# Optimization experiments

Measured on AMD Instinct MI355X. Metric: run time of the kernel, lower is better.

Reference implementation:

```python
import jax, jax.numpy as jnp
import numpy as np


def conv1x1(x, w, b):
    # x: (B,C,H,W), w: (O,C), b: (O,)
    return jnp.einsum('bchw,oc->bohw', x, w) + b[None, :, None, None]


def maxpool2x2(x):
    B, C, H, W = x.shape
    return x.reshape(B, C, H // 2, 2, W // 2, 2).max(axis=(3, 5))


def setup_inputs() -> dict:
    key = jax.random.key(0)
    ks = jax.random.split(key, 10)
    B, C, H, W = 16, 256, 64, 64
    K = 8
    ck, ch = C // K, C // 2  # 32, 128
    sc = lambda fan_in: 1.0 / np.sqrt(fan_in)
    return {
        'x': jax.random.normal(ks[0], (B, C, H, W), jnp.float32),
        'wf': jax.random.normal(ks[1], (ck, C), jnp.float32) * sc(C),
        'bf': jnp.zeros((ck,), jnp.float32),
        'wg': jax.random.normal(ks[2], (ck, C), jnp.float32) * sc(C),
        'bg': jnp.zeros((ck,), jnp.float32),
        'wh': jax.random.normal(ks[3], (ch, C), jnp.float32) * sc(C),
        'bh': jnp.zeros((ch,), jnp.float32),
        'wv': jax.random.normal(ks[4], (C, ch), jnp.float32) * sc(ch),
        'bv': jnp.zeros((C,), jnp.float32),
        'gamma': jnp.float32(0.5),  # nonzero so the attention branch matters
    }


def reference(x, wf, bf, wg, bg, wh, bh, wv, bv, gamma):
    B, C, H, W = x.shape
    HW = H * W
    f = conv1x1(x, wf, bf).reshape(B, -1, HW)            # (B, C/K, HW)
    g = maxpool2x2(conv1x1(x, wg, bg))                    # (B, C/K, H/2, W/2)
    h = maxpool2x2(conv1x1(x, wh, bh))                    # (B, C/2, H/2, W/2)
    HWp = HW // 4
    g = g.reshape(B, -1, HWp)
    h = h.reshape(B, -1, HWp)
    s = jnp.einsum('bck,bcl->bkl', f, g)                  # (B, HW, HW')
    beta = jax.nn.softmax(s, axis=-1)
    o = jnp.einsum('bjk,blk->bjl', h, beta)               # (B, C/2, HW)
    o = o.reshape(B, -1, H, W)
    return gamma * conv1x1(o, wv, bv) + x
```

## Files before the change

kernel.cpp:

```cpp
#include <hip/hip_runtime.h>
#include <hip/hip_bf16.h>
#include <stdint.h>

#define B_N   16
#define C_N   256
#define W_N   64
#define HW_N  4096
#define CK_N  32
#define CH_N  128
#define HWP_N 1024
#define MR_N  192

typedef __attribute__((ext_vector_type(8))) short short8;
typedef __attribute__((ext_vector_type(4))) float f32x4;
typedef __attribute__((ext_vector_type(4))) unsigned uint4v;

#define MFMA(a, b, c) __builtin_amdgcn_mfma_f32_16x16x32_bf16((a), (b), (c), 0, 0, 0)

__device__ __forceinline__ unsigned short f2bf(float f) {
    union { float f; unsigned u; } v; v.f = f;
    unsigned r = v.u + 0x7FFFu + ((v.u >> 16) & 1u);
    return (unsigned short)(r >> 16);
}
__device__ __forceinline__ unsigned packrn(float lo, float hi) {
    unsigned a = __float_as_uint(lo) + 0x8000u;
    unsigned b = __float_as_uint(hi) + 0x8000u;
    return __builtin_amdgcn_perm(b, a, 0x07060302);
}
__device__ __forceinline__ short8 ld8(const void* p) {
    return *reinterpret_cast<const short8*>(p);
}

__global__ __launch_bounds__(256) void k_prep(
    const float* __restrict__ wf, const float* __restrict__ wg,
    const float* __restrict__ wh, const float* __restrict__ wv,
    unsigned short* __restrict__ Wc, unsigned short* __restrict__ Wv)
{
    int i = blockIdx.x * 256 + threadIdx.x;
    if (i < MR_N * C_N) {
        int r = i / C_N, c = i % C_N;
        float v = (r < 32) ? wf[r * C_N + c]
                : (r < 64) ? wg[(r - 32) * C_N + c]
                           : wh[(r - 64) * C_N + c];
        Wc[i] = f2bf(v);
    }
    if (i < C_N * CH_N) Wv[i] = f2bf(wv[i]);
}

__global__ __launch_bounds__(256) void k_conv_fgh(
    const float* __restrict__ x, const unsigned short* __restrict__ Wc,
    const float* __restrict__ bfp, const float* __restrict__ bgp, const float* __restrict__ bhp,
    unsigned short* __restrict__ f_, unsigned short* __restrict__ g_, unsigned short* __restrict__ h_)
{
    __shared__ __align__(16) unsigned char lds[64 * 512];
    const int T = threadIdx.x;
    const int lane = T & 63, wid = T >> 6;
    const int blk = blockIdx.x;
    const int b = blk >> 6;
    const int seg = blk & 63;
    const int rp = seg >> 1;
    const int half = seg & 1;
    const float* xb = x + (size_t)b * C_N * HW_N;

    #pragma unroll
    for (int i = 0; i < 8; ++i) {
        int task = i * 256 + T;
        int pq = task & 15;
        int cp = task >> 4;
        int px0 = pq * 4;
        int row = 2 * rp + (px0 >> 5);
        int wcol = half * 32 + (px0 & 31);
        const float4 v0 = *reinterpret_cast<const float4*>(xb + (size_t)(2 * cp) * HW_N + row * W_N + wcol);
        const float4 v1 = *reinterpret_cast<const float4*>(xb + (size_t)(2 * cp + 1) * HW_N + row * W_N + wcol);
        float vlo[4] = {v0.x, v0.y, v0.z, v0.w};
        float vhi[4] = {v1.x, v1.y, v1.z, v1.w};
        int kc = cp >> 2, co = cp & 3;
        #pragma unroll
        for (int j = 0; j < 4; ++j) {
            int px = px0 + j;
            *reinterpret_cast<unsigned*>(lds + px * 512 + ((kc ^ (px & 31)) << 4) + co * 4)
                = packrn(vlo[j], vhi[j]);
        }
    }
    __syncthreads();

    const int l15 = lane & 15, quad = lane >> 4;
    f32x4 acc[3][4];
    #pragma unroll
    for (int mt = 0; mt < 3; ++mt)
        #pragma unroll
        for (int nt = 0; nt < 4; ++nt)
            acc[mt][nt] = f32x4{0.f, 0.f, 0.f, 0.f};

    const int m0base = wid * 48;
    for (int k0 = 0; k0 < 256; k0 += 32) {
        short8 afr[3];
        #pragma unroll
        for (int mt = 0; mt < 3; ++mt)
            afr[mt] = ld8(Wc + (size_t)(m0base + mt * 16 + l15) * C_N + k0 + quad * 8);
        #pragma unroll
        for (int nt = 0; nt < 4; ++nt) {
            int px = nt * 16 + l15;
            int kc = (k0 >> 3) + quad;
            short8 bfr = ld8(lds + px * 512 + ((kc ^ (px & 31)) << 4));
            #pragma unroll
            for (int mt = 0; mt < 3; ++mt)
                acc[mt][nt] = MFMA(afr[mt], bfr, acc[mt][nt]);
        }
    }

    #pragma unroll
    for (int mt = 0; mt < 3; ++mt) {
        int mbase = m0base + mt * 16;
        int mrow0 = mbase + quad * 4;
        float bias[4];
        #pragma unroll
        for (int r = 0; r < 4; ++r) {
            int m = mrow0 + r;
            bias[r] = (m < 32) ? bfp[m] : (m < 64) ? bgp[m - 32] : bhp[m - 64];
        }
        if (mbase < 32) {
            #pragma unroll
            for (int nt = 0; nt < 4; ++nt) {
                int px = nt * 16 + l15;
                int p = (2 * rp + (px >> 5)) * W_N + half * 32 + (px & 31);
                uint2 u;
                u.x = packrn(acc[mt][nt][0] + bias[0], acc[mt][nt][1] + bias[1]);
                u.y = packrn(acc[mt][nt][2] + bias[2], acc[mt][nt][3] + bias[3]);
                *reinterpret_cast<uint2*>(f_ + ((size_t)b * HW_N + p) * CK_N + mrow0) = u;
            }
        } else if (mbase < 64) {
            int gc0 = mrow0 - 32;
            #pragma unroll
            for (int nt = 0; nt < 2; ++nt) {
                float pv[4];
                #pragma unroll
                for (int r = 0; r < 4; ++r) {
                    float m1 = fmaxf(acc[mt][nt][r], acc[mt][nt + 2][r]);
                    pv[r] = fmaxf(m1, __shfl_xor(m1, 1)) + bias[r];
                }
                if ((lane & 1) == 0) {
                    int kp = rp * 32 + half * 16 + ((nt * 16 + l15) >> 1);
                    uint2 u;
                    u.x = packrn(pv[0], pv[1]);
                    u.y = packrn(pv[2], pv[3]);
                    *reinterpret_cast<uint2*>(g_ + ((size_t)b * HWP_N + kp) * CK_N + gc0) = u;
                }
            }
        } else {
            int hc0 = mrow0 - 64;
            #pragma unroll
            for (int nt = 0; nt < 2; ++nt) {
                float pv[4];
                #pragma unroll
                for (int r = 0; r < 4; ++r) {
                    float m1 = fmaxf(acc[mt][nt][r], acc[mt][nt + 2][r]);
                    pv[r] = fmaxf(m1, __shfl_xor(m1, 1)) + bias[r];
                }
                #pragma unroll
                for (int r = 0; r < 4; ++r) {
                    int lo = (int)(packrn(pv[r], pv[r]) & 0xFFFFu);
                    int hi = __shfl_down(lo, 2);
                    if ((lane & 3) == 0) {
                        int kp2 = rp * 32 + half * 16 + nt * 8 + (l15 >> 1);
                        *reinterpret_cast<unsigned*>(
                            h_ + ((size_t)b * CH_N + hc0 + r) * HWP_N + kp2)
                            = (unsigned)lo | ((unsigned)hi << 16);
                    }
                }
            }
        }
    }
}

__global__ __launch_bounds__(256, 4) void k_attn(
    const unsigned short* __restrict__ f_, const unsigned short* __restrict__ g_,
    const unsigned short* __restrict__ h_, const unsigned short* __restrict__ Wv,
    const float* __restrict__ bv, const float* __restrict__ x,
    const float* __restrict__ gamma_p, float* __restrict__ out)
{
    __shared__ __align__(16) unsigned char Vl[2 * 17408];
    const int T = threadIdx.x;
    const int lane = T & 63, wid = T >> 6;
    const int l15 = lane & 15, quad = lane >> 4;

    const int blk = blockIdx.x;
    const int b = blk >> 6;
    const int q0w = (blk & 63) * 64 + wid * 16;
    const unsigned short* fb = f_ + (size_t)b * HW_N * CK_N;
    const unsigned short* gb = g_ + (size_t)b * HWP_N * CK_N;
    const unsigned short* hb = h_ + (size_t)b * CH_N * HWP_N;

    short8 ffr = ld8(fb + (size_t)(q0w + l15) * CK_N + quad * 8);

    const f32x4 zf = {0.f, 0.f, 0.f, 0.f};
    f32x4 oacc[8];
    #pragma unroll
    for (int ct = 0; ct < 8; ++ct)
        oacc[ct] = f32x4{0.f, 0.f, 0.f, 0.f};
    float lsum = 0.f;

    const int sch = T >> 3, skq = T & 7;
    const int kq = ((l15 >> 2) << 3) | (l15 & 3);

    uint4 vpre[4];
    #pragma unroll
    for (int i = 0; i < 4; ++i)
        vpre[i] = *reinterpret_cast<const uint4*>(hb + (size_t)(sch + i * 32) * HWP_N + skq * 8);
    short8 gcur[4];
    #pragma unroll
    for (int kt = 0; kt < 4; ++kt)
        gcur[kt] = ld8(gb + (size_t)(((kt >> 1) << 5) + ((kt & 1) << 2) + kq) * CK_N + quad * 8);

    for (int c = 0; c < 16; ++c) {
        unsigned char* buf = Vl + (c & 1) * 17408;
        #pragma unroll
        for (int i = 0; i < 4; ++i) {
            unsigned char* dst = buf + (sch + i * 32) * 136 + skq * 16;
            *reinterpret_cast<uint2*>(dst)     = uint2{vpre[i].x, vpre[i].y};
            *reinterpret_cast<uint2*>(dst + 8) = uint2{vpre[i].z, vpre[i].w};
        }
        if (c < 15) {
            #pragma unroll
            for (int i = 0; i < 4; ++i)
                vpre[i] = *reinterpret_cast<const uint4*>(
                    hb + (size_t)(sch + i * 32) * HWP_N + (c + 1) * 64 + skq * 8);
        }
        __syncthreads();

        f32x4 sp[4];
        #pragma unroll
        for (int kt = 0; kt < 4; ++kt)
            sp[kt] = MFMA(gcur[kt], ffr, zf);
        if (c < 15) {
            #pragma unroll
            for (int kt = 0; kt < 4; ++kt)
                gcur[kt] = ld8(gb + (size_t)((c + 1) * 64 + ((kt >> 1) << 5) + ((kt & 1) << 2) + kq) * CK_N + quad * 8);
        }

        unsigned pw[8];
        float lw = 0.f;
        #pragma unroll
        for (int kt = 0; kt < 4; ++kt) {
            float p0 = __builtin_amdgcn_exp2f(sp[kt][0] * 1.44269504f - 28.85390082f);
            float p1 = __builtin_amdgcn_exp2f(sp[kt][1] * 1.44269504f - 28.85390082f);
            float p2 = __builtin_amdgcn_exp2f(sp[kt][2] * 1.44269504f - 28.85390082f);
            float p3 = __builtin_amdgcn_exp2f(sp[kt][3] * 1.44269504f - 28.85390082f);
            lw += (p0 + p1) + (p2 + p3);
            pw[2 * kt]     = packrn(p0, p1);
            pw[2 * kt + 1] = packrn(p2, p3);
        }
        lsum += lw;
        short8 pfA = __builtin_bit_cast(short8, uint4v{pw[0], pw[1], pw[2], pw[3]});
        short8 pfB = __builtin_bit_cast(short8, uint4v{pw[4], pw[5], pw[6], pw[7]});

        const int vbase = l15 * 136 + quad * 16;
        #pragma unroll
        for (int ct = 0; ct < 8; ++ct) {
            const unsigned char* p = buf + vbase + ct * 2176;
            uint2 aLo0 = *reinterpret_cast<const uint2*>(p);
            uint2 aLo1 = *reinterpret_cast<const uint2*>(p + 8);
            short8 a0 = __builtin_bit_cast(short8, uint4v{aLo0.x, aLo0.y, aLo1.x, aLo1.y});
            oacc[ct] = MFMA(a0, pfA, oacc[ct]);
            uint2 aHi0 = *reinterpret_cast<const uint2*>(p + 64);
            uint2 aHi1 = *reinterpret_cast<const uint2*>(p + 72);
            short8 a1 = __builtin_bit_cast(short8, uint4v{aHi0.x, aHi0.y, aHi1.x, aHi1.y});
            oacc[ct] = MFMA(a1, pfB, oacc[ct]);
        }
    }

    lsum += __shfl_xor(lsum, 16); lsum += __shfl_xor(lsum, 32);
    const float rl = 1.f / lsum;

    unsigned char* o_lds = Vl;
    {
        const int row = wid * 16 + l15;
        #pragma unroll
        for (int ct = 0; ct < 8; ++ct) {
            uint2 u;
            u.x = packrn(oacc[ct][0] * rl, oacc[ct][1] * rl);
            u.y = packrn(oacc[ct][2] * rl, oacc[ct][3] * rl);
            *reinterpret_cast<uint2*>(o_lds + row * 264 + (ct * 16 + quad * 4) * 2) = u;
        }
    }
    __syncthreads();

    const int pxb = (blk & 63) * 64;
    const int oc0 = wid * 64;
    f32x4 acc2[4][4];
    #pragma unroll
    for (int mt = 0; mt < 4; ++mt)
        #pragma unroll
        for (int nt = 0; nt < 4; ++nt)
            acc2[mt][nt] = f32x4{0.f, 0.f, 0.f, 0.f};

    #pragma unroll
    for (int k0 = 0; k0 < 128; k0 += 32) {
        short8 ofr[4];
        #pragma unroll
        for (int nt = 0; nt < 4; ++nt) {
            const unsigned char* p = o_lds + (nt * 16 + l15) * 264 + k0 * 2 + quad * 16;
            uint2 a0 = *reinterpret_cast<const uint2*>(p);
            uint2 a1 = *reinterpret_cast<const uint2*>(p + 8);
            ofr[nt] = __builtin_bit_cast(short8, uint4v{a0.x, a0.y, a1.x, a1.y});
        }
        #pragma unroll
        for (int mt = 0; mt < 4; ++mt) {
            short8 wfr = ld8(Wv + (size_t)(oc0 + mt * 16 + l15) * CH_N + k0 + quad * 8);
            #pragma unroll
            for (int nt = 0; nt < 4; ++nt)
                acc2[mt][nt] = MFMA(ofr[nt], wfr, acc2[mt][nt]);
        }
    }

    const float gamma = *gamma_p;
    const float* xb = x + (size_t)b * C_N * HW_N;
    float* outb = out + (size_t)b * C_N * HW_N;
    #pragma unroll
    for (int mt = 0; mt < 4; ++mt) {
        int oc = oc0 + mt * 16 + l15;
        float bvv = bv[oc];
        #pragma unroll
        for (int nt = 0; nt < 4; ++nt) {
            size_t base = (size_t)oc * HW_N + pxb + nt * 16 + quad * 4;
            float4 xv = *reinterpret_cast<const float4*>(xb + base);
            float4 ov;
            ov.x = gamma * (acc2[mt][nt][0] + bvv) + xv.x;
            ov.y = gamma * (acc2[mt][nt][1] + bvv) + xv.y;
            ov.z = gamma * (acc2[mt][nt][2] + bvv) + xv.z;
            ov.w = gamma * (acc2[mt][nt][3] + bvv) + xv.w;
            *reinterpret_cast<float4*>(outb + base) = ov;
        }
    }
}

extern "C" void kernel_launch(void* const* d_in, const int* in_sizes, int n_in,
                              void* d_out, int out_size, void* d_ws, size_t ws_size,
                              hipStream_t stream) {
    const float* x     = (const float*)d_in[0];
    const float* wf    = (const float*)d_in[1];
    const float* bf    = (const float*)d_in[2];
    const float* wg    = (const float*)d_in[3];
    const float* bg    = (const float*)d_in[4];
    const float* wh    = (const float*)d_in[5];
    const float* bh    = (const float*)d_in[6];
    const float* wv    = (const float*)d_in[7];
    const float* bv    = (const float*)d_in[8];
    const float* gamma = (const float*)d_in[9];
    float* out = (float*)d_out;
    char* ws = (char*)d_ws;

    unsigned short* f_ = (unsigned short*)(ws);
    unsigned short* g_ = (unsigned short*)(ws + 4194304);
    unsigned short* h_ = (unsigned short*)(ws + 5242880);
    unsigned short* Wc = (unsigned short*)(ws + 26214400);
    unsigned short* Wv = (unsigned short*)(ws + 26312704);

    k_prep<<<192, 256, 0, stream>>>(wf, wg, wh, wv, Wc, Wv);
    k_conv_fgh<<<1024, 256, 0, stream>>>(x, Wc, bf, bg, bh, f_, g_, h_);
    k_attn<<<1024, 256, 0, stream>>>(f_, g_, h_, Wv, bv, x, gamma, out);
}
```

Baseline: 182.7 us.

## Permute V rows in LDS so output stays in registers for final conv

The V tile rows are written to LDS in a permuted order so that each wave's MFMA output accumulators already form the B-operand layout needed for the final 1x1 conv. This removes the LDS round-trip and block barrier used to transpose the attention output, and each wave now computes all 256 output channels for its own 16 pixels directly from registers. In exchange, the epilogue uses scalar 4-byte global loads and stores strided by channel instead of float4 accesses, and each wave reloads the full Wv matrix.

```diff
diff --git a/kernel.cpp b/kernel.cpp
--- a/kernel.cpp
+++ b/kernel.cpp
@@ -201,6 +201,7 @@
     float lsum = 0.f;
 
     const int sch = T >> 3, skq = T & 7;
+    const int rho0 = ((sch >> 2) & 1) * 16 + (sch >> 3) * 4 + (sch & 3);
     const int kq = ((l15 >> 2) << 3) | (l15 & 3);
 
     uint4 vpre[4];
@@ -216,7 +217,7 @@
         unsigned char* buf = Vl + (c & 1) * 17408;
         #pragma unroll
         for (int i = 0; i < 4; ++i) {
-            unsigned char* dst = buf + (sch + i * 32) * 136 + skq * 16;
+            unsigned char* dst = buf + (rho0 + i * 32) * 136 + skq * 16;
             *reinterpret_cast<uint2*>(dst)     = uint2{vpre[i].x, vpre[i].y};
             *reinterpret_cast<uint2*>(dst + 8) = uint2{vpre[i].z, vpre[i].w};
         }
@@ -272,64 +273,34 @@
     lsum += __shfl_xor(lsum, 16); lsum += __shfl_xor(lsum, 32);
     const float rl = 1.f / lsum;
 
-    unsigned char* o_lds = Vl;
-    {
-        const int row = wid * 16 + l15;
-        #pragma unroll
-        for (int ct = 0; ct < 8; ++ct) {
-            uint2 u;
-            u.x = packrn(oacc[ct][0] * rl, oacc[ct][1] * rl);
-            u.y = packrn(oacc[ct][2] * rl, oacc[ct][3] * rl);
-            *reinterpret_cast<uint2*>(o_lds + row * 264 + (ct * 16 + quad * 4) * 2) = u;
-        }
-    }
-    __syncthreads();
-
-    const int pxb = (blk & 63) * 64;
-    const int oc0 = wid * 64;
-    f32x4 acc2[4][4];
-    #pragma unroll
-    for (int mt = 0; mt < 4; ++mt)
-        #pragma unroll
-        for (int nt = 0; nt < 4; ++nt)
-            acc2[mt][nt] = f32x4{0.f, 0.f, 0.f, 0.f};
-
-    #pragma unroll
-    for (int k0 = 0; k0 < 128; k0 += 32) {
-        short8 ofr[4];
-        #pragma unroll
-        for (int nt = 0; nt < 4; ++nt) {
-            const unsigned char* p = o_lds + (nt * 16 + l15) * 264 + k0 * 2 + quad * 16;
-            uint2 a0 = *reinterpret_cast<const uint2*>(p);
-            uint2 a1 = *reinterpret_cast<const uint2*>(p + 8);
-            ofr[nt] = __builtin_bit_cast(short8, uint4v{a0.x, a0.y, a1.x, a1.y});
-        }
-        #pragma unroll
-        for (int mt = 0; mt < 4; ++mt) {
-            short8 wfr = ld8(Wv + (size_t)(oc0 + mt * 16 + l15) * CH_N + k0 + quad * 8);
-            #pragma unroll
-            for (int nt = 0; nt < 4; ++nt)
-                acc2[mt][nt] = MFMA(ofr[nt], wfr, acc2[mt][nt]);
-        }
+    short8 pfO[4];
+    #pragma unroll
+    for (int t = 0; t < 4; ++t) {
+        uint4v u;
+        u.x = packrn(oacc[2 * t][0] * rl,     oacc[2 * t][1] * rl);
+        u.y = packrn(oacc[2 * t][2] * rl,     oacc[2 * t][3] * rl);
+        u.z = packrn(oacc[2 * t + 1][0] * rl, oacc[2 * t + 1][1] * rl);
+        u.w = packrn(oacc[2 * t + 1][2] * rl, oacc[2 * t + 1][3] * rl);
+        pfO[t] = __builtin_bit_cast(short8, u);
     }
 
     const float gamma = *gamma_p;
     const float* xb = x + (size_t)b * C_N * HW_N;
     float* outb = out + (size_t)b * C_N * HW_N;
-    #pragma unroll
-    for (int mt = 0; mt < 4; ++mt) {
-        int oc = oc0 + mt * 16 + l15;
-        float bvv = bv[oc];
-        #pragma unroll
-        for (int nt = 0; nt < 4; ++nt) {
-            size_t base = (size_t)oc * HW_N + pxb + nt * 16 + quad * 4;
-            float4 xv = *reinterpret_cast<const float4*>(xb + base);
-            float4 ov;
-            ov.x = gamma * (acc2[mt][nt][0] + bvv) + xv.x;
-            ov.y = gamma * (acc2[mt][nt][1] + bvv) + xv.y;
-            ov.z = gamma * (acc2[mt][nt][2] + bvv) + xv.z;
-            ov.w = gamma * (acc2[mt][nt][3] + bvv) + xv.w;
-            *reinterpret_cast<float4*>(outb + base) = ov;
+    const int q = q0w + l15;
+    #pragma unroll
+    for (int ot = 0; ot < 16; ++ot) {
+        f32x4 acc = zf;
+        #pragma unroll
+        for (int t = 0; t < 4; ++t) {
+            short8 wfr = ld8(Wv + (size_t)(ot * 16 + l15) * CH_N + t * 32 + quad * 8);
+            acc = MFMA(wfr, pfO[t], acc);
+        }
+        #pragma unroll
+        for (int r = 0; r < 4; ++r) {
+            int oc = ot * 16 + quad * 4 + r;
+            size_t idx = (size_t)oc * HW_N + q;
+            outb[idx] = gamma * (acc[r] + bv[oc]) + xb[idx];
         }
     }
 }
```

After: 195.7 us. 7.1% more time.
